# Performance work log

Measured on AMD Instinct MI355X. Metric: run time of the kernel, lower is better.

## Reference

```python
import jax, jax.numpy as jnp
from jax import lax
import numpy as np

T, B, I, H, OUT = 1024, 32, 128, 512, 10


def _lstm_layer(x, W_ih, W_hh, b):
    """PyTorch-convention LSTM layer. x: [T,B,in], W_ih: [4H,in], W_hh: [4H,H], b: [4H].
    Gate order: i, f, g, o. Returns all hidden states [T,B,H]."""
    hdim = W_hh.shape[1]
    # Precompute input projections for all timesteps (big GEMM, compute-bound).
    x_proj = jnp.einsum('tbi,gi->tbg', x, W_ih) + b  # [T,B,4H]

    def step(carry, xp_t):
        h, c = carry
        gates = xp_t + h @ W_hh.T  # [B,4H]
        i_g, f_g, g_g, o_g = jnp.split(gates, 4, axis=-1)
        i_g = jax.nn.sigmoid(i_g)
        f_g = jax.nn.sigmoid(f_g)
        g_g = jnp.tanh(g_g)
        o_g = jax.nn.sigmoid(o_g)
        c = f_g * c + i_g * g_g
        h = o_g * jnp.tanh(c)
        return (h, c), h

    h0 = jnp.zeros((x.shape[1], hdim), x.dtype)
    c0 = jnp.zeros((x.shape[1], hdim), x.dtype)
    _, hs = lax.scan(step, (h0, c0), x_proj)
    return hs  # [T,B,H]


def setup_inputs() -> dict:
    key = jax.random.key(0)
    ks = jax.random.split(key, 9)
    s1 = 1.0 / np.sqrt(H)  # PyTorch LSTM init scale U(-1/sqrt(H), 1/sqrt(H)); use scaled normal
    return {
        'data': jax.random.normal(ks[0], (T, B, I), jnp.float32),
        'W_ih1': jax.random.normal(ks[1], (4 * H, I), jnp.float32) * s1,
        'W_hh1': jax.random.normal(ks[2], (4 * H, H), jnp.float32) * s1,
        'b1': jax.random.normal(ks[3], (4 * H,), jnp.float32) * s1,
        'W_ih2': jax.random.normal(ks[4], (4 * H, H), jnp.float32) * s1,
        'W_hh2': jax.random.normal(ks[5], (4 * H, H), jnp.float32) * s1,
        'b2': jax.random.normal(ks[6], (4 * H,), jnp.float32) * s1,
        'W3': jax.random.normal(ks[7], (OUT, H), jnp.float32) * s1,
        'b3': jax.random.normal(ks[8], (OUT,), jnp.float32) * s1,
    }


def reference(data, W_ih1, W_hh1, b1, W_ih2, W_hh2, b2, W3, b3):
    h = _lstm_layer(data, W_ih1, W_hh1, b1)   # [T,B,H]
    h = _lstm_layer(h, W_ih2, W_hh2, b2)      # [T,B,H]
    logits = jnp.einsum('tbh,oh->tbo', h, W3) + b3  # [T,B,OUT]
    return jax.nn.softmax(logits, axis=2)
```

## Files before the change

kernel.cpp:

```cpp
#include <hip/hip_runtime.h>
#include <cstdint>
#include <cstddef>

#define TCHUNK 128
#define NCHUNK 8
#define BATCH 32
#define IDIM 128
#define HDIM 512
#define GDIM 2048
#define ODIM 10
#define NBLK 256
#define XPSTEP (GDIM * BATCH)
#define SLAB_F 16384
#define SLAB_B (SLAB_F * 4)

typedef float f4 __attribute__((ext_vector_type(4)));
typedef float f2 __attribute__((ext_vector_type(2)));

__device__ __forceinline__ void llc_store(float* p, float v) {
  asm volatile("global_store_dword %0, %1, off sc0 sc1" :: "v"(p), "v"(v) : "memory");
}
__device__ __forceinline__ float quad_sum(float x) {
  int t = __builtin_amdgcn_update_dpp(0, __float_as_int(x), 0xB1, 0xF, 0xF, true);
  x += __int_as_float(t);
  t = __builtin_amdgcn_update_dpp(0, __float_as_int(x), 0x4E, 0xF, 0xF, true);
  x += __int_as_float(t);
  return x;
}

#define BARRIER() do {                                                      \
    asm volatile("s_waitcnt lgkmcnt(0)" ::: "memory");                      \
    __builtin_amdgcn_sched_barrier(0);                                      \
    __builtin_amdgcn_s_barrier();                                           \
    __builtin_amdgcn_sched_barrier(0);                                      \
  } while (0)

template<int K>
__launch_bounds__(256, 2)
__global__ void proj_kernel(const float* __restrict__ X,
                            const float* __restrict__ W,
                            const float* __restrict__ bias,
                            float* __restrict__ P) {
  __shared__ float Xs[8][132];
  __shared__ float Ws[8][132];
  const int tid = threadIdx.x;
  const int n0 = blockIdx.x * 128;
  const int m0 = blockIdx.y * 128;
  const int tx = tid & 15, ty = tid >> 4;
  const int lm = tid >> 1;
  const int kq = (tid & 1) * 4;
  f2 acc2[8][4];
#pragma unroll
  for (int i = 0; i < 8; ++i)
#pragma unroll
    for (int j = 0; j < 4; ++j) acc2[i][j] = (f2){0.f, 0.f};

  for (int k0 = 0; k0 < K; k0 += 8) {
    const float4 xv = *(const float4*)&X[(size_t)(m0 + lm) * K + k0 + kq];
    const float4 wv = *(const float4*)&W[(size_t)(n0 + lm) * K + k0 + kq];
    __syncthreads();
    Xs[kq + 0][lm] = xv.x; Xs[kq + 1][lm] = xv.y; Xs[kq + 2][lm] = xv.z; Xs[kq + 3][lm] = xv.w;
    Ws[kq + 0][lm] = wv.x; Ws[kq + 1][lm] = wv.y; Ws[kq + 2][lm] = wv.z; Ws[kq + 3][lm] = wv.w;
    __syncthreads();
#pragma unroll
    for (int kk = 0; kk < 8; ++kk) {
      float a[8];
      *(float4*)&a[0] = *(const float4*)&Xs[kk][ty * 8];
      *(float4*)&a[4] = *(const float4*)&Xs[kk][ty * 8 + 4];
      f2 b2[4];
#pragma unroll
      for (int jp = 0; jp < 4; ++jp) b2[jp] = *(const f2*)&Ws[kk][tx * 8 + 2 * jp];
#pragma unroll
      for (int i = 0; i < 8; ++i)
#pragma unroll
        for (int jp = 0; jp < 4; ++jp) acc2[i][jp] += b2[jp] * a[i];
    }
  }
  const int mb = m0 + ty * 8;
  const int t  = mb >> 5;
  const int b0 = mb & 31;
#pragma unroll
  for (int j = 0; j < 8; ++j) {
    const int n = n0 + tx * 8 + j;
    const float bj = bias[n];
    float* dst = &P[((size_t)t * GDIM + n) * BATCH + b0];
#pragma unroll
    for (int i = 0; i < 8; ++i)
      dst[i] = ((j & 1) ? acc2[i][j >> 1].y : acc2[i][j >> 1].x) + bj;
  }
}

__launch_bounds__(256, 1)
__global__ void scan_kernel(const float* __restrict__ xp,
                            const float* __restrict__ Whh,
                            float* __restrict__ hout,
                            float* __restrict__ hb,
                            float* __restrict__ ccur,
                            int first) {
  __shared__ float h_s[2112];
  __shared__ float red[1024];
  __shared__ float gate_s[256];
  __shared__ float pad[17408];

  const int tid = threadIdx.x, bid = blockIdx.x;
  const int g = bid & 7, rank = bid >> 3, slot16 = rank * 16;
  const int w = tid >> 6, l = tid & 63;
  const int s4 = l & 3, rq = l >> 2;
  const int sg = 4 * w + s4;
  const int cx = sg & 7;
  const int kb = 32 * sg;

  float wreg[4][32];
#pragma unroll
  for (int r = 0; r < 4; ++r) {
    const int rl = 4 * rq + r;
    const float* wp = Whh + (size_t)((rl >> 4) * HDIM + slot16 + (rl & 15)) * HDIM + kb;
#pragma unroll
    for (int e = 0; e < 32; ++e) wreg[r][e] = wp[e ^ cx];
  }

  const int cl = l >> 4, m = l & 15;
  const int sgS = 4 * w + (m >> 2);
  const int sig = sgS & 7;
  int dsaddr[8];
#pragma unroll
  for (int i = 0; i < 8; ++i)
    dsaddr[i] = 132 * sgS + 4 * (8 * (m & 3) + (i ^ sig)) + cl;
  const int srcoff = cl * 512 + 128 * w + 8 * m;

  const int qg = tid >> 6, jg = (tid >> 2) & 15, bg = tid & 3;
  const float* xq = xp + (size_t)(qg * HDIM + slot16 + jg) * BATCH + g * 4 + bg;

  const int jj = l >> 2, bb = l & 3;

  float c_st = 0.f;
  if (!first && w == 0) c_st = ccur[(size_t)(g * 4 + bb) * HDIM + slot16 + jj];

  const float* hptr = &h_s[132 * sg];

#pragma unroll 1
  for (int tt = 0; tt < TCHUNK; ++tt) {
    const float* src = hb + (size_t)tt * SLAB_F + g * 2048 + srcoff;
    f4 va, vb;
    int guard = 0;
    while (true) {
      asm volatile("global_load_dwordx4 %0, %2, off sc0 sc1\n\t"
                   "global_load_dwordx4 %1, %3, off sc0 sc1\n\t"
                   "s_waitcnt vmcnt(0)"
                   : "=&v"(va), "=&v"(vb) : "v"(src), "v"(src + 4) : "memory");
      const bool ok =
          __float_as_uint(va.x) != 0xFFFFFFFFu && __float_as_uint(va.y) != 0xFFFFFFFFu &&
          __float_as_uint(va.z) != 0xFFFFFFFFu && __float_as_uint(va.w) != 0xFFFFFFFFu &&
          __float_as_uint(vb.x) != 0xFFFFFFFFu && __float_as_uint(vb.y) != 0xFFFFFFFFu &&
          __float_as_uint(vb.z) != 0xFFFFFFFFu && __float_as_uint(vb.w) != 0xFFFFFFFFu;
      if (__all(ok) || ++guard > 100000) break;
      __builtin_amdgcn_s_sleep(1);
    }
    h_s[dsaddr[0]] = va.x; h_s[dsaddr[1]] = va.y;
    h_s[dsaddr[2]] = va.z; h_s[dsaddr[3]] = va.w;
    h_s[dsaddr[4]] = vb.x; h_s[dsaddr[5]] = vb.y;
    h_s[dsaddr[6]] = vb.z; h_s[dsaddr[7]] = vb.w;
    const float xpv = xq[(size_t)tt * XPSTEP];
    BARRIER();

    f2 a01[4], a23[4];
#pragma unroll
    for (int r = 0; r < 4; ++r) { a01[r] = (f2){0.f, 0.f}; a23[r] = (f2){0.f, 0.f}; }
#pragma unroll
    for (int kk = 0; kk < 32; ++kk) {
      const f4 hv = *(const f4*)&hptr[4 * kk];
      const f2 h01 = {hv.x, hv.y}, h23 = {hv.z, hv.w};
#pragma unroll
      for (int r = 0; r < 4; ++r) {
        a01[r] += h01 * wreg[r][kk];
        a23[r] += h23 * wreg[r][kk];
      }
    }
#pragma unroll
    for (int r = 0; r < 4; ++r) {
      a01[r].x = quad_sum(a01[r].x); a01[r].y = quad_sum(a01[r].y);
      a23[r].x = quad_sum(a23[r].x); a23[r].y = quad_sum(a23[r].y);
    }
    f2 r01, r23;
    { const f2 v0 = (s4 & 1) ? a01[1] : a01[0];
      const f2 v1 = (s4 & 1) ? a01[3] : a01[2];
      r01 = (s4 & 2) ? v1 : v0;
      const f2 u0 = (s4 & 1) ? a23[1] : a23[0];
      const f2 u1 = (s4 & 1) ? a23[3] : a23[2];
      r23 = (s4 & 2) ? u1 : u0; }
    *(f4*)&red[(w << 8) + 4 * l] = (f4){r01.x, r01.y, r23.x, r23.y};
    BARRIER();

    const float pre = red[tid] + red[256 + tid] + red[512 + tid] + red[768 + tid] + xpv;
    gate_s[tid] = (qg == 2) ? tanhf(pre) : 1.f / (1.f + __expf(-pre));
    BARRIER();

    if (w == 0) {
      const float ig = gate_s[jj * 4 + bb];
      const float fg = gate_s[64 + jj * 4 + bb];
      const float gg = gate_s[128 + jj * 4 + bb];
      const float og = gate_s[192 + jj * 4 + bb];
      c_st = fg * c_st + ig * gg;
      const float hval = og * tanhf(c_st);
      llc_store(hb + (size_t)(tt + 1) * SLAB_F + g * 2048 + bb * 512 + slot16 + jj, hval);
      hout[(size_t)tt * (BATCH * HDIM) + (size_t)(g * 4 + bb) * HDIM + slot16 + jj] = hval;
    }
  }
  if (w == 0) ccur[(size_t)(g * 4 + bb) * HDIM + slot16 + jj] = c_st;
  ((volatile float*)pad)[tid] = c_st;
}

__launch_bounds__(256, 2)
__global__ void head_kernel(const float* __restrict__ h2,
                            const float* __restrict__ W3,
                            const float* __restrict__ b3,
                            float* __restrict__ outp) {
  const int tid = threadIdx.x;
  const int lane = tid & 63;
  const int wv = tid >> 6;
  const int row = blockIdx.x * 4 + wv;
  const float* hrow = &h2[(size_t)row * HDIM];
  float hreg[8];
  *(float4*)&hreg[0] = *(const float4*)&hrow[lane * 8];
  *(float4*)&hreg[4] = *(const float4*)&hrow[lane * 8 + 4];
  float logit[ODIM];
#pragma unroll
  for (int o = 0; o < ODIM; ++o) {
    const float* wrow = &W3[o * HDIM + lane * 8];
    float w[8];
    *(float4*)&w[0] = *(const float4*)&wrow[0];
    *(float4*)&w[4] = *(const float4*)&wrow[4];
    float pp = 0.f;
#pragma unroll
    for (int j = 0; j < 8; ++j) pp += hreg[j] * w[j];
#pragma unroll
    for (int off = 32; off > 0; off >>= 1) pp += __shfl_xor(pp, off);
    logit[o] = pp + b3[o];
  }
  float mx = logit[0];
#pragma unroll
  for (int o = 1; o < ODIM; ++o) mx = fmaxf(mx, logit[o]);
  float ssum = 0.f;
#pragma unroll
  for (int o = 0; o < ODIM; ++o) { logit[o] = __expf(logit[o] - mx); ssum += logit[o]; }
  const float inv = 1.f / ssum;
  if (lane == 0) {
    float* dst = &outp[(size_t)row * ODIM];
#pragma unroll
    for (int o = 0; o < ODIM; ++o) dst[o] = logit[o] * inv;
  }
}

extern "C" void kernel_launch(void* const* d_in, const int* in_sizes, int n_in,
                              void* d_out, int out_size, void* d_ws, size_t ws_size,
                              hipStream_t stream) {
  const float* data  = (const float*)d_in[0];
  const float* W_ih1 = (const float*)d_in[1];
  const float* W_hh1 = (const float*)d_in[2];
  const float* b1    = (const float*)d_in[3];
  const float* W_ih2 = (const float*)d_in[4];
  const float* W_hh2 = (const float*)d_in[5];
  const float* b2    = (const float*)d_in[6];
  const float* W3    = (const float*)d_in[7];
  const float* b3    = (const float*)d_in[8];
  float* outp = (float*)d_out;

  char* ws = (char*)d_ws;
  size_t off = 0;
  float* xp    = (float*)(ws + off); off += (size_t)TCHUNK * GDIM * BATCH * 4;
  float* h1c   = (float*)(ws + off); off += (size_t)TCHUNK * BATCH * HDIM * 4;
  float* h2c   = (float*)(ws + off); off += (size_t)TCHUNK * BATCH * HDIM * 4;
  float* hb1   = (float*)(ws + off); off += (size_t)(TCHUNK + 1) * SLAB_B;
  float* hb2   = (float*)(ws + off); off += (size_t)(TCHUNK + 1) * SLAB_B;
  float* ccur1 = (float*)(ws + off); off += BATCH * HDIM * 4;
  float* ccur2 = (float*)(ws + off); off += BATCH * HDIM * 4;
  if (off > ws_size) return;

  hipMemsetAsync(hb1, 0x00, SLAB_B, stream);
  hipMemsetAsync((char*)hb1 + SLAB_B, 0xFF, (size_t)TCHUNK * SLAB_B, stream);
  hipMemsetAsync(hb2, 0x00, SLAB_B, stream);
  hipMemsetAsync((char*)hb2 + SLAB_B, 0xFF, (size_t)TCHUNK * SLAB_B, stream);

  const dim3 pgrid(GDIM / 128, (TCHUNK * BATCH) / 128);
  for (int c = 0; c < NCHUNK; ++c) {
    const float* xin = data + (size_t)c * TCHUNK * BATCH * IDIM;
    proj_kernel<IDIM><<<pgrid, 256, 0, stream>>>(xin, W_ih1, b1, xp);
    scan_kernel<<<NBLK, 256, 0, stream>>>(xp, W_hh1, h1c, hb1, ccur1, c == 0);
    if (c < NCHUNK - 1) {
      hipMemcpyAsync(hb1, (char*)hb1 + (size_t)TCHUNK * SLAB_B, SLAB_B,
                     hipMemcpyDeviceToDevice, stream);
      hipMemsetAsync((char*)hb1 + SLAB_B, 0xFF, (size_t)TCHUNK * SLAB_B, stream);
    }
    proj_kernel<HDIM><<<pgrid, 256, 0, stream>>>(h1c, W_ih2, b2, xp);
    scan_kernel<<<NBLK, 256, 0, stream>>>(xp, W_hh2, h2c, hb2, ccur2, c == 0);
    if (c < NCHUNK - 1) {
      hipMemcpyAsync(hb2, (char*)hb2 + (size_t)TCHUNK * SLAB_B, SLAB_B,
                     hipMemcpyDeviceToDevice, stream);
      hipMemsetAsync((char*)hb2 + SLAB_B, 0xFF, (size_t)TCHUNK * SLAB_B, stream);
    }
    head_kernel<<<(TCHUNK * BATCH) / 4, 256, 0, stream>>>(
        h2c, W3, b3, outp + (size_t)c * TCHUNK * BATCH * ODIM);
  }
}
```

Before: 8.744 ms.

## Wavefront-pipeline both LSTM layers in one fused persistent scan kernel

Merges the two layer scans into one templated kernel that runs layer 1 on chunk c+1 and layer 2 on chunk c in the same timestep loop. Both layers share the barriers and the polling latency of each serial step. The chunk length is halved so the pipeline fill and drain are shorter, and a second xp buffer lets both projections stay live at once. In exchange each CU holds twice the recurrent weights in registers and does two dot phases per step, and there are more kernel launches and recycle memsets.

```diff
diff --git a/kernel.cpp b/kernel.cpp
--- a/kernel.cpp
+++ b/kernel.cpp
@@ -2,8 +2,8 @@
 #include <cstdint>
 #include <cstddef>
 
-#define TCHUNK 128
-#define NCHUNK 8
+#define TCHUNK 64
+#define NCHUNK 16
 #define BATCH 32
 #define IDIM 128
 #define HDIM 512
@@ -34,6 +34,11 @@
     __builtin_amdgcn_s_barrier();                                           \
     __builtin_amdgcn_sched_barrier(0);                                      \
   } while (0)
+
+#define SENT_OK(v) (__float_as_uint(v.x) != 0xFFFFFFFFu && \
+                    __float_as_uint(v.y) != 0xFFFFFFFFu && \
+                    __float_as_uint(v.z) != 0xFFFFFFFFu && \
+                    __float_as_uint(v.w) != 0xFFFFFFFFu)
 
 template<int K>
 __launch_bounds__(256, 2)
@@ -90,17 +95,21 @@
   }
 }
 
+template<bool L1, bool L2>
 __launch_bounds__(256, 1)
-__global__ void scan_kernel(const float* __restrict__ xp,
-                            const float* __restrict__ Whh,
-                            float* __restrict__ hout,
-                            float* __restrict__ hb,
-                            float* __restrict__ ccur,
-                            int first) {
-  __shared__ float h_s[2112];
-  __shared__ float red[1024];
-  __shared__ float gate_s[256];
-  __shared__ float pad[17408];
+__global__ void scan_pair(const float* __restrict__ xpA, const float* __restrict__ WhhA,
+                          float* __restrict__ houtA, float* __restrict__ hbA,
+                          float* __restrict__ ccurA, int firstA,
+                          const float* __restrict__ xpB, const float* __restrict__ WhhB,
+                          float* __restrict__ houtB, float* __restrict__ hbB,
+                          float* __restrict__ ccurB, int firstB) {
+  __shared__ float h_s1[2112];
+  __shared__ float h_s2[2112];
+  __shared__ float red1[1024];
+  __shared__ float red2[1024];
+  __shared__ float gate1[256];
+  __shared__ float gate2[256];
+  __shared__ float pad[13952];
 
   const int tid = threadIdx.x, bid = blockIdx.x;
   const int g = bid & 7, rank = bid >> 3, slot16 = rank * 16;
@@ -110,13 +119,24 @@
   const int cx = sg & 7;
   const int kb = 32 * sg;
 
-  float wreg[4][32];
-#pragma unroll
-  for (int r = 0; r < 4; ++r) {
-    const int rl = 4 * rq + r;
-    const float* wp = Whh + (size_t)((rl >> 4) * HDIM + slot16 + (rl & 15)) * HDIM + kb;
-#pragma unroll
-    for (int e = 0; e < 32; ++e) wreg[r][e] = wp[e ^ cx];
+  float wregA[4][32], wregB[4][32];
+  if constexpr (L1) {
+#pragma unroll
+    for (int r = 0; r < 4; ++r) {
+      const int rl = 4 * rq + r;
+      const float* wp = WhhA + (size_t)((rl >> 4) * HDIM + slot16 + (rl & 15)) * HDIM + kb;
+#pragma unroll
+      for (int e = 0; e < 32; ++e) wregA[r][e] = wp[e ^ cx];
+    }
+  }
+  if constexpr (L2) {
+#pragma unroll
+    for (int r = 0; r < 4; ++r) {
+      const int rl = 4 * rq + r;
+      const float* wp = WhhB + (size_t)((rl >> 4) * HDIM + slot16 + (rl & 15)) * HDIM + kb;
+#pragma unroll
+      for (int e = 0; e < 32; ++e) wregB[r][e] = wp[e ^ cx];
+    }
   }
 
   const int cl = l >> 4, m = l & 15;
@@ -129,85 +149,143 @@
   const int srcoff = cl * 512 + 128 * w + 8 * m;
 
   const int qg = tid >> 6, jg = (tid >> 2) & 15, bg = tid & 3;
-  const float* xq = xp + (size_t)(qg * HDIM + slot16 + jg) * BATCH + g * 4 + bg;
+  const size_t xqo = (size_t)(qg * HDIM + slot16 + jg) * BATCH + g * 4 + bg;
 
   const int jj = l >> 2, bb = l & 3;
-
-  float c_st = 0.f;
-  if (!first && w == 0) c_st = ccur[(size_t)(g * 4 + bb) * HDIM + slot16 + jj];
-
-  const float* hptr = &h_s[132 * sg];
+  const size_t cco = (size_t)(g * 4 + bb) * HDIM + slot16 + jj;
+
+  float cA = 0.f, cB = 0.f;
+  if (w == 0) {
+    if (L1 && !firstA) cA = ccurA[cco];
+    if (L2 && !firstB) cB = ccurB[cco];
+  }
+
+  const float* hp1 = &h_s1[132 * sg];
+  const float* hp2 = &h_s2[132 * sg];
 
 #pragma unroll 1
   for (int tt = 0; tt < TCHUNK; ++tt) {
-    const float* src = hb + (size_t)tt * SLAB_F + g * 2048 + srcoff;
-    f4 va, vb;
+    const float* s1 = hbA + (size_t)tt * SLAB_F + g * 2048 + srcoff;
+    const float* s2 = hbB + (size_t)tt * SLAB_F + g * 2048 + srcoff;
+    f4 va1, vb1, va2, vb2;
     int guard = 0;
     while (true) {
-      asm volatile("global_load_dwordx4 %0, %2, off sc0 sc1\n\t"
-                   "global_load_dwordx4 %1, %3, off sc0 sc1\n\t"
-                   "s_waitcnt vmcnt(0)"
-                   : "=&v"(va), "=&v"(vb) : "v"(src), "v"(src + 4) : "memory");
-      const bool ok =
-          __float_as_uint(va.x) != 0xFFFFFFFFu && __float_as_uint(va.y) != 0xFFFFFFFFu &&
-          __float_as_uint(va.z) != 0xFFFFFFFFu && __float_as_uint(va.w) != 0xFFFFFFFFu &&
-          __float_as_uint(vb.x) != 0xFFFFFFFFu && __float_as_uint(vb.y) != 0xFFFFFFFFu &&
-          __float_as_uint(vb.z) != 0xFFFFFFFFu && __float_as_uint(vb.w) != 0xFFFFFFFFu;
-      if (__all(ok) || ++guard > 100000) break;
+      bool ok;
+      if constexpr (L1 && L2) {
+        asm volatile("global_load_dwordx4 %0, %4, off sc0 sc1\n\t"
+                     "global_load_dwordx4 %1, %5, off sc0 sc1\n\t"
+                     "global_load_dwordx4 %2, %6, off sc0 sc1\n\t"
+                     "global_load_dwordx4 %3, %7, off sc0 sc1\n\t"
+                     "s_waitcnt vmcnt(0)"
+                     : "=&v"(va1), "=&v"(vb1), "=&v"(va2), "=&v"(vb2)
+                     : "v"(s1), "v"(s1 + 4), "v"(s2), "v"(s2 + 4) : "memory");
+        ok = SENT_OK(va1) && SENT_OK(vb1) && SENT_OK(va2) && SENT_OK(vb2);
+      } else if constexpr (L1) {
+        asm volatile("global_load_dwordx4 %0, %2, off sc0 sc1\n\t"
+                     "global_load_dwordx4 %1, %3, off sc0 sc1\n\t"
+                     "s_waitcnt vmcnt(0)"
+                     : "=&v"(va1), "=&v"(vb1) : "v"(s1), "v"(s1 + 4) : "memory");
+        ok = SENT_OK(va1) && SENT_OK(vb1);
+      } else {
+        asm volatile("global_load_dwordx4 %0, %2, off sc0 sc1\n\t"
+                     "global_load_dwordx4 %1, %3, off sc0 sc1\n\t"
+                     "s_waitcnt vmcnt(0)"
+                     : "=&v"(va2), "=&v"(vb2) : "v"(s2), "v"(s2 + 4) : "memory");
+        ok = SENT_OK(va2) && SENT_OK(vb2);
+      }
+      if (__all(ok) || ++guard > 200000) break;
       __builtin_amdgcn_s_sleep(1);
     }
-    h_s[dsaddr[0]] = va.x; h_s[dsaddr[1]] = va.y;
-    h_s[dsaddr[2]] = va.z; h_s[dsaddr[3]] = va.w;
-    h_s[dsaddr[4]] = vb.x; h_s[dsaddr[5]] = vb.y;
-    h_s[dsaddr[6]] = vb.z; h_s[dsaddr[7]] = vb.w;
-    const float xpv = xq[(size_t)tt * XPSTEP];
+    if constexpr (L1) {
+      h_s1[dsaddr[0]] = va1.x; h_s1[dsaddr[1]] = va1.y;
+      h_s1[dsaddr[2]] = va1.z; h_s1[dsaddr[3]] = va1.w;
+      h_s1[dsaddr[4]] = vb1.x; h_s1[dsaddr[5]] = vb1.y;
+      h_s1[dsaddr[6]] = vb1.z; h_s1[dsaddr[7]] = vb1.w;
+    }
+    if constexpr (L2) {
+      h_s2[dsaddr[0]] = va2.x; h_s2[dsaddr[1]] = va2.y;
+      h_s2[dsaddr[2]] = va2.z; h_s2[dsaddr[3]] = va2.w;
+      h_s2[dsaddr[4]] = vb2.x; h_s2[dsaddr[5]] = vb2.y;
+      h_s2[dsaddr[6]] = vb2.z; h_s2[dsaddr[7]] = vb2.w;
+    }
+    float xpv1 = 0.f, xpv2 = 0.f;
+    if constexpr (L1) xpv1 = xpA[(size_t)tt * XPSTEP + xqo];
+    if constexpr (L2) xpv2 = xpB[(size_t)tt * XPSTEP + xqo];
     BARRIER();
 
-    f2 a01[4], a23[4];
-#pragma unroll
-    for (int r = 0; r < 4; ++r) { a01[r] = (f2){0.f, 0.f}; a23[r] = (f2){0.f, 0.f}; }
-#pragma unroll
-    for (int kk = 0; kk < 32; ++kk) {
-      const f4 hv = *(const f4*)&hptr[4 * kk];
-      const f2 h01 = {hv.x, hv.y}, h23 = {hv.z, hv.w};
-#pragma unroll
-      for (int r = 0; r < 4; ++r) {
-        a01[r] += h01 * wreg[r][kk];
-        a23[r] += h23 * wreg[r][kk];
+#define DOT_PHASE(HPTR, WREG, RED)                                          \
+    {                                                                       \
+      f2 a01[4], a23[4];                                                    \
+      _Pragma("unroll")                                                     \
+      for (int r = 0; r < 4; ++r) { a01[r] = (f2){0.f,0.f}; a23[r] = (f2){0.f,0.f}; } \
+      _Pragma("unroll")                                                     \
+      for (int kk = 0; kk < 32; ++kk) {                                     \
+        const f4 hv = *(const f4*)&HPTR[4 * kk];                            \
+        const f2 h01 = {hv.x, hv.y}, h23 = {hv.z, hv.w};                    \
+        _Pragma("unroll")                                                   \
+        for (int r = 0; r < 4; ++r) {                                       \
+          a01[r] += h01 * WREG[r][kk];                                      \
+          a23[r] += h23 * WREG[r][kk];                                      \
+        }                                                                   \
+      }                                                                     \
+      _Pragma("unroll")                                                     \
+      for (int r = 0; r < 4; ++r) {                                         \
+        a01[r].x = quad_sum(a01[r].x); a01[r].y = quad_sum(a01[r].y);       \
+        a23[r].x = quad_sum(a23[r].x); a23[r].y = quad_sum(a23[r].y);       \
+      }                                                                     \
+      f2 r01, r23;                                                          \
+      { const f2 v0 = (s4 & 1) ? a01[1] : a01[0];                           \
+        const f2 v1 = (s4 & 1) ? a01[3] : a01[2];                           \
+        r01 = (s4 & 2) ? v1 : v0;                                           \
+        const f2 u0 = (s4 & 1) ? a23[1] : a23[0];                           \
+        const f2 u1 = (s4 & 1) ? a23[3] : a23[2];                           \
+        r23 = (s4 & 2) ? u1 : u0; }                                         \
+      *(f4*)&RED[(w << 8) + 4 * l] = (f4){r01.x, r01.y, r23.x, r23.y};      \
+    }
+
+    if constexpr (L1) DOT_PHASE(hp1, wregA, red1)
+    if constexpr (L2) DOT_PHASE(hp2, wregB, red2)
+    BARRIER();
+
+    if constexpr (L1) {
+      const float pre = red1[tid] + red1[256 + tid] + red1[512 + tid] + red1[768 + tid] + xpv1;
+      gate1[tid] = (qg == 2) ? tanhf(pre) : 1.f / (1.f + __expf(-pre));
+    }
+    if constexpr (L2) {
+      const float pre = red2[tid] + red2[256 + tid] + red2[512 + tid] + red2[768 + tid] + xpv2;
+      gate2[tid] = (qg == 2) ? tanhf(pre) : 1.f / (1.f + __expf(-pre));
+    }
+    BARRIER();
+
+    if (w == 0) {
+      if constexpr (L1) {
+        const float ig = gate1[jj * 4 + bb];
+        const float fg = gate1[64 + jj * 4 + bb];
+        const float gg = gate1[128 + jj * 4 + bb];
+        const float og = gate1[192 + jj * 4 + bb];
+        cA = fg * cA + ig * gg;
+        const float hval = og * tanhf(cA);
+        llc_store(hbA + (size_t)(tt + 1) * SLAB_F + g * 2048 + bb * 512 + slot16 + jj, hval);
+        houtA[(size_t)tt * (BATCH * HDIM) + cco] = hval;
       }
-    }
-#pragma unroll
-    for (int r = 0; r < 4; ++r) {
-      a01[r].x = quad_sum(a01[r].x); a01[r].y = quad_sum(a01[r].y);
-      a23[r].x = quad_sum(a23[r].x); a23[r].y = quad_sum(a23[r].y);
-    }
-    f2 r01, r23;
-    { const f2 v0 = (s4 & 1) ? a01[1] : a01[0];
-      const f2 v1 = (s4 & 1) ? a01[3] : a01[2];
-      r01 = (s4 & 2) ? v1 : v0;
-      const f2 u0 = (s4 & 1) ? a23[1] : a23[0];
-      const f2 u1 = (s4 & 1) ? a23[3] : a23[2];
-      r23 = (s4 & 2) ? u1 : u0; }
-    *(f4*)&red[(w << 8) + 4 * l] = (f4){r01.x, r01.y, r23.x, r23.y};
-    BARRIER();
-
-    const float pre = red[tid] + red[256 + tid] + red[512 + tid] + red[768 + tid] + xpv;
-    gate_s[tid] = (qg == 2) ? tanhf(pre) : 1.f / (1.f + __expf(-pre));
-    BARRIER();
-
-    if (w == 0) {
-      const float ig = gate_s[jj * 4 + bb];
-      const float fg = gate_s[64 + jj * 4 + bb];
-      const float gg = gate_s[128 + jj * 4 + bb];
-      const float og = gate_s[192 + jj * 4 + bb];
-      c_st = fg * c_st + ig * gg;
-      const float hval = og * tanhf(c_st);
-      llc_store(hb + (size_t)(tt + 1) * SLAB_F + g * 2048 + bb * 512 + slot16 + jj, hval);
-      hout[(size_t)tt * (BATCH * HDIM) + (size_t)(g * 4 + bb) * HDIM + slot16 + jj] = hval;
-    }
-  }
-  if (w == 0) ccur[(size_t)(g * 4 + bb) * HDIM + slot16 + jj] = c_st;
-  ((volatile float*)pad)[tid] = c_st;
+      if constexpr (L2) {
+        const float ig = gate2[jj * 4 + bb];
+        const float fg = gate2[64 + jj * 4 + bb];
+        const float gg = gate2[128 + jj * 4 + bb];
+        const float og = gate2[192 + jj * 4 + bb];
+        cB = fg * cB + ig * gg;
+        const float hval = og * tanhf(cB);
+        llc_store(hbB + (size_t)(tt + 1) * SLAB_F + g * 2048 + bb * 512 + slot16 + jj, hval);
+        houtB[(size_t)tt * (BATCH * HDIM) + cco] = hval;
+      }
+    }
+#undef DOT_PHASE
+  }
+  if (w == 0) {
+    if constexpr (L1) ccurA[cco] = cA;
+    if constexpr (L2) ccurB[cco] = cB;
+  }
+  ((volatile float*)pad)[tid] = cA + cB;
 }
 
 __launch_bounds__(256, 2)
@@ -267,7 +345,8 @@
 
   char* ws = (char*)d_ws;
   size_t off = 0;
-  float* xp    = (float*)(ws + off); off += (size_t)TCHUNK * GDIM * BATCH * 4;
+  float* xp1   = (float*)(ws + off); off += (size_t)TCHUNK * GDIM * BATCH * 4;
+  float* xp2   = (float*)(ws + off); off += (size_t)TCHUNK * GDIM * BATCH * 4;
   float* h1c   = (float*)(ws + off); off += (size_t)TCHUNK * BATCH * HDIM * 4;
   float* h2c   = (float*)(ws + off); off += (size_t)TCHUNK * BATCH * HDIM * 4;
   float* hb1   = (float*)(ws + off); off += (size_t)(TCHUNK + 1) * SLAB_B;
@@ -282,23 +361,38 @@
   hipMemsetAsync((char*)hb2 + SLAB_B, 0xFF, (size_t)TCHUNK * SLAB_B, stream);
 
   const dim3 pgrid(GDIM / 128, (TCHUNK * BATCH) / 128);
-  for (int c = 0; c < NCHUNK; ++c) {
-    const float* xin = data + (size_t)c * TCHUNK * BATCH * IDIM;
-    proj_kernel<IDIM><<<pgrid, 256, 0, stream>>>(xin, W_ih1, b1, xp);
-    scan_kernel<<<NBLK, 256, 0, stream>>>(xp, W_hh1, h1c, hb1, ccur1, c == 0);
-    if (c < NCHUNK - 1) {
-      hipMemcpyAsync(hb1, (char*)hb1 + (size_t)TCHUNK * SLAB_B, SLAB_B,
-                     hipMemcpyDeviceToDevice, stream);
-      hipMemsetAsync((char*)hb1 + SLAB_B, 0xFF, (size_t)TCHUNK * SLAB_B, stream);
-    }
-    proj_kernel<HDIM><<<pgrid, 256, 0, stream>>>(h1c, W_ih2, b2, xp);
-    scan_kernel<<<NBLK, 256, 0, stream>>>(xp, W_hh2, h2c, hb2, ccur2, c == 0);
-    if (c < NCHUNK - 1) {
-      hipMemcpyAsync(hb2, (char*)hb2 + (size_t)TCHUNK * SLAB_B, SLAB_B,
-                     hipMemcpyDeviceToDevice, stream);
-      hipMemsetAsync((char*)hb2 + SLAB_B, 0xFF, (size_t)TCHUNK * SLAB_B, stream);
-    }
+
+#define RECYCLE(HB) do {                                                    \
+    hipMemcpyAsync(HB, (char*)HB + (size_t)TCHUNK * SLAB_B, SLAB_B,         \
+                   hipMemcpyDeviceToDevice, stream);                        \
+    hipMemsetAsync((char*)HB + SLAB_B, 0xFF, (size_t)TCHUNK * SLAB_B, stream); \
+  } while (0)
+
+  proj_kernel<IDIM><<<pgrid, 256, 0, stream>>>(data, W_ih1, b1, xp1);
+  scan_pair<true, false><<<NBLK, 256, 0, stream>>>(
+      xp1, W_hh1, h1c, hb1, ccur1, 1, xp2, W_hh2, h2c, hb2, ccur2, 1);
+  RECYCLE(hb1);
+  proj_kernel<HDIM><<<pgrid, 256, 0, stream>>>(h1c, W_ih2, b2, xp2);
+  proj_kernel<IDIM><<<pgrid, 256, 0, stream>>>(
+      data + (size_t)TCHUNK * BATCH * IDIM, W_ih1, b1, xp1);
+
+  for (int c = 0; c < NCHUNK - 1; ++c) {
+    scan_pair<true, true><<<NBLK, 256, 0, stream>>>(
+        xp1, W_hh1, h1c, hb1, ccur1, 0,
+        xp2, W_hh2, h2c, hb2, ccur2, c == 0);
     head_kernel<<<(TCHUNK * BATCH) / 4, 256, 0, stream>>>(
         h2c, W3, b3, outp + (size_t)c * TCHUNK * BATCH * ODIM);
-  }
-}
+    RECYCLE(hb1);
+    RECYCLE(hb2);
+    proj_kernel<HDIM><<<pgrid, 256, 0, stream>>>(h1c, W_ih2, b2, xp2);
+    if (c + 2 < NCHUNK)
+      proj_kernel<IDIM><<<pgrid, 256, 0, stream>>>(
+          data + (size_t)(c + 2) * TCHUNK * BATCH * IDIM, W_ih1, b1, xp1);
+  }
+
+  scan_pair<false, true><<<NBLK, 256, 0, stream>>>(
+      xp1, W_hh1, h1c, hb1, ccur1, 0, xp2, W_hh2, h2c, hb2, ccur2, 0);
+  head_kernel<<<(TCHUNK * BATCH) / 4, 256, 0, stream>>>(
+      h2c, W3, b3, outp + (size_t)(NCHUNK - 1) * TCHUNK * BATCH * ODIM);
+#undef RECYCLE
+}
```

New measurement: 13.75 ms. 1.57x slower.

## Wavefront-pipeline both LSTM layers in one split scan kernel

Applied to the files above, without the earlier changes.

Merges the two layer scans into one launch. Layer 2 processes chunk s-1 while layer 1 processes chunk s, each on half the blocks (128 per layer). Each block now owns 32 hidden units and holds twice as many recurrent weights in registers. The chunk size is halved to shorten the pipeline fill. The aim is to overlap the two serial recurrences and roughly halve the total serial step count. The cost is twice the per-block dot-product work per step, much higher register pressure, and more launches and memset/copy traffic per chunk.

```diff
diff --git a/kernel.cpp b/kernel.cpp
--- a/kernel.cpp
+++ b/kernel.cpp
@@ -2,8 +2,8 @@
 #include <cstdint>
 #include <cstddef>
 
-#define TCHUNK 128
-#define NCHUNK 8
+#define TCHUNK 64
+#define NCHUNK 16
 #define BATCH 32
 #define IDIM 128
 #define HDIM 512
@@ -91,32 +91,45 @@
 }
 
 __launch_bounds__(256, 1)
-__global__ void scan_kernel(const float* __restrict__ xp,
-                            const float* __restrict__ Whh,
-                            float* __restrict__ hout,
-                            float* __restrict__ hb,
-                            float* __restrict__ ccur,
-                            int first) {
+__global__ void scan_split(const float* __restrict__ xp1, const float* __restrict__ Whh1,
+                           float* __restrict__ hout1, float* __restrict__ hb1,
+                           float* __restrict__ ccur1, int first1, int act1,
+                           const float* __restrict__ xp2, const float* __restrict__ Whh2,
+                           float* __restrict__ hout2, float* __restrict__ hb2,
+                           float* __restrict__ ccur2, int first2, int act2) {
   __shared__ float h_s[2112];
-  __shared__ float red[1024];
-  __shared__ float gate_s[256];
-  __shared__ float pad[17408];
-
-  const int tid = threadIdx.x, bid = blockIdx.x;
-  const int g = bid & 7, rank = bid >> 3, slot16 = rank * 16;
+  __shared__ float red[2048];
+  __shared__ float gate_s[512];
+  __shared__ float pad[15872];
+
+  const int bid = blockIdx.x;
+  const int lay = bid >> 7;
+  if (!(lay ? act2 : act1)) return;
+  const float* xp  = lay ? xp2  : xp1;
+  const float* Whh = lay ? Whh2 : Whh1;
+  float* hout = lay ? hout2 : hout1;
+  float* hb   = lay ? hb2   : hb1;
+  float* ccur = lay ? ccur2 : ccur1;
+  const int first = lay ? first2 : first1;
+
+  const int tid = threadIdx.x;
+  const int bidl = bid & 127;
+  const int g = bidl & 7, rank = bidl >> 3, slot32 = rank * 32;
   const int w = tid >> 6, l = tid & 63;
   const int s4 = l & 3, rq = l >> 2;
   const int sg = 4 * w + s4;
   const int cx = sg & 7;
   const int kb = 32 * sg;
 
-  float wreg[4][32];
+  float wA[4][32], wB[4][32];
 #pragma unroll
   for (int r = 0; r < 4; ++r) {
     const int rl = 4 * rq + r;
-    const float* wp = Whh + (size_t)((rl >> 4) * HDIM + slot16 + (rl & 15)) * HDIM + kb;
-#pragma unroll
-    for (int e = 0; e < 32; ++e) wreg[r][e] = wp[e ^ cx];
+    const int s = rl & 31;
+    const float* wpA = Whh + (size_t)((rl >> 5) * HDIM + slot32 + s) * HDIM + kb;
+    const float* wpB = Whh + (size_t)((2 + (rl >> 5)) * HDIM + slot32 + s) * HDIM + kb;
+#pragma unroll
+    for (int e = 0; e < 32; ++e) { wA[r][e] = wpA[e ^ cx]; wB[r][e] = wpB[e ^ cx]; }
   }
 
   const int cl = l >> 4, m = l & 15;
@@ -128,13 +141,17 @@
     dsaddr[i] = 132 * sgS + 4 * (8 * (m & 3) + (i ^ sig)) + cl;
   const int srcoff = cl * 512 + 128 * w + 8 * m;
 
-  const int qg = tid >> 6, jg = (tid >> 2) & 15, bg = tid & 3;
-  const float* xq = xp + (size_t)(qg * HDIM + slot16 + jg) * BATCH + g * 4 + bg;
-
-  const int jj = l >> 2, bb = l & 3;
+  const int rowA = tid >> 2, chn = tid & 3;
+  const size_t xqoA = (size_t)((rowA >> 5) * HDIM + slot32 + (rowA & 31)) * BATCH
+                      + g * 4 + chn;
+  const size_t xqoB = xqoA + (size_t)2 * HDIM * BATCH;
+
+  const int uj = ((w << 6) + l) >> 2;
+  const int ub = l & 3;
+  const size_t cco = (size_t)(g * 4 + ub) * HDIM + slot32 + uj;
 
   float c_st = 0.f;
-  if (!first && w == 0) c_st = ccur[(size_t)(g * 4 + bb) * HDIM + slot16 + jj];
+  if (!first && w < 2) c_st = ccur[cco];
 
   const float* hptr = &h_s[132 * sg];
 
@@ -153,60 +170,73 @@
           __float_as_uint(va.z) != 0xFFFFFFFFu && __float_as_uint(va.w) != 0xFFFFFFFFu &&
           __float_as_uint(vb.x) != 0xFFFFFFFFu && __float_as_uint(vb.y) != 0xFFFFFFFFu &&
           __float_as_uint(vb.z) != 0xFFFFFFFFu && __float_as_uint(vb.w) != 0xFFFFFFFFu;
-      if (__all(ok) || ++guard > 100000) break;
+      if (__all(ok) || ++guard > 200000) break;
       __builtin_amdgcn_s_sleep(1);
     }
     h_s[dsaddr[0]] = va.x; h_s[dsaddr[1]] = va.y;
     h_s[dsaddr[2]] = va.z; h_s[dsaddr[3]] = va.w;
     h_s[dsaddr[4]] = vb.x; h_s[dsaddr[5]] = vb.y;
     h_s[dsaddr[6]] = vb.z; h_s[dsaddr[7]] = vb.w;
-    const float xpv = xq[(size_t)tt * XPSTEP];
+    const float xpvA = xp[(size_t)tt * XPSTEP + xqoA];
+    const float xpvB = xp[(size_t)tt * XPSTEP + xqoB];
     BARRIER();
 
-    f2 a01[4], a23[4];
-#pragma unroll
-    for (int r = 0; r < 4; ++r) { a01[r] = (f2){0.f, 0.f}; a23[r] = (f2){0.f, 0.f}; }
-#pragma unroll
-    for (int kk = 0; kk < 32; ++kk) {
-      const f4 hv = *(const f4*)&hptr[4 * kk];
-      const f2 h01 = {hv.x, hv.y}, h23 = {hv.z, hv.w};
-#pragma unroll
-      for (int r = 0; r < 4; ++r) {
-        a01[r] += h01 * wreg[r][kk];
-        a23[r] += h23 * wreg[r][kk];
-      }
-    }
-#pragma unroll
-    for (int r = 0; r < 4; ++r) {
-      a01[r].x = quad_sum(a01[r].x); a01[r].y = quad_sum(a01[r].y);
-      a23[r].x = quad_sum(a23[r].x); a23[r].y = quad_sum(a23[r].y);
-    }
-    f2 r01, r23;
-    { const f2 v0 = (s4 & 1) ? a01[1] : a01[0];
-      const f2 v1 = (s4 & 1) ? a01[3] : a01[2];
-      r01 = (s4 & 2) ? v1 : v0;
-      const f2 u0 = (s4 & 1) ? a23[1] : a23[0];
-      const f2 u1 = (s4 & 1) ? a23[3] : a23[2];
-      r23 = (s4 & 2) ? u1 : u0; }
-    *(f4*)&red[(w << 8) + 4 * l] = (f4){r01.x, r01.y, r23.x, r23.y};
+#define DOT_BANK(WREG, ROFF)                                                \
+    {                                                                       \
+      f2 a01[4], a23[4];                                                    \
+      _Pragma("unroll")                                                     \
+      for (int r = 0; r < 4; ++r) { a01[r] = (f2){0.f,0.f}; a23[r] = (f2){0.f,0.f}; } \
+      _Pragma("unroll")                                                     \
+      for (int kk = 0; kk < 32; ++kk) {                                     \
+        const f4 hv = *(const f4*)&hptr[4 * kk];                            \
+        const f2 h01 = {hv.x, hv.y}, h23 = {hv.z, hv.w};                    \
+        _Pragma("unroll")                                                   \
+        for (int r = 0; r < 4; ++r) {                                       \
+          a01[r] += h01 * WREG[r][kk];                                      \
+          a23[r] += h23 * WREG[r][kk];                                      \
+        }                                                                   \
+      }                                                                     \
+      _Pragma("unroll")                                                     \
+      for (int r = 0; r < 4; ++r) {                                         \
+        a01[r].x = quad_sum(a01[r].x); a01[r].y = quad_sum(a01[r].y);       \
+        a23[r].x = quad_sum(a23[r].x); a23[r].y = quad_sum(a23[r].y);       \
+      }                                                                     \
+      f2 r01, r23;                                                          \
+      { const f2 v0 = (s4 & 1) ? a01[1] : a01[0];                           \
+        const f2 v1 = (s4 & 1) ? a01[3] : a01[2];                           \
+        r01 = (s4 & 2) ? v1 : v0;                                           \
+        const f2 u0 = (s4 & 1) ? a23[1] : a23[0];                           \
+        const f2 u1 = (s4 & 1) ? a23[3] : a23[2];                           \
+        r23 = (s4 & 2) ? u1 : u0; }                                         \
+      *(f4*)&red[(ROFF) + (w << 8) + 4 * l] = (f4){r01.x, r01.y, r23.x, r23.y}; \
+    }
+    DOT_BANK(wA, 0)
+    DOT_BANK(wB, 1024)
+#undef DOT_BANK
     BARRIER();
 
-    const float pre = red[tid] + red[256 + tid] + red[512 + tid] + red[768 + tid] + xpv;
-    gate_s[tid] = (qg == 2) ? tanhf(pre) : 1.f / (1.f + __expf(-pre));
+    {
+      const float preA = red[tid] + red[256 + tid] + red[512 + tid] + red[768 + tid] + xpvA;
+      gate_s[tid] = 1.f / (1.f + __expf(-preA));
+      const float preB = red[1024 + tid] + red[1280 + tid] + red[1536 + tid]
+                       + red[1792 + tid] + xpvB;
+      gate_s[256 + tid] = (tid < 128) ? tanhf(preB)
+                                      : 1.f / (1.f + __expf(-preB));
+    }
     BARRIER();
 
-    if (w == 0) {
-      const float ig = gate_s[jj * 4 + bb];
-      const float fg = gate_s[64 + jj * 4 + bb];
-      const float gg = gate_s[128 + jj * 4 + bb];
-      const float og = gate_s[192 + jj * 4 + bb];
+    if (w < 2) {
+      const float ig = gate_s[uj * 4 + ub];
+      const float fg = gate_s[128 + uj * 4 + ub];
+      const float gg = gate_s[256 + uj * 4 + ub];
+      const float og = gate_s[384 + uj * 4 + ub];
       c_st = fg * c_st + ig * gg;
       const float hval = og * tanhf(c_st);
-      llc_store(hb + (size_t)(tt + 1) * SLAB_F + g * 2048 + bb * 512 + slot16 + jj, hval);
-      hout[(size_t)tt * (BATCH * HDIM) + (size_t)(g * 4 + bb) * HDIM + slot16 + jj] = hval;
-    }
-  }
-  if (w == 0) ccur[(size_t)(g * 4 + bb) * HDIM + slot16 + jj] = c_st;
+      llc_store(hb + (size_t)(tt + 1) * SLAB_F + g * 2048 + ub * 512 + slot32 + uj, hval);
+      hout[(size_t)tt * (BATCH * HDIM) + cco] = hval;
+    }
+  }
+  if (w < 2) ccur[cco] = c_st;
   ((volatile float*)pad)[tid] = c_st;
 }
 
@@ -267,7 +297,8 @@
 
   char* ws = (char*)d_ws;
   size_t off = 0;
-  float* xp    = (float*)(ws + off); off += (size_t)TCHUNK * GDIM * BATCH * 4;
+  float* xp1   = (float*)(ws + off); off += (size_t)TCHUNK * GDIM * BATCH * 4;
+  float* xp2   = (float*)(ws + off); off += (size_t)TCHUNK * GDIM * BATCH * 4;
   float* h1c   = (float*)(ws + off); off += (size_t)TCHUNK * BATCH * HDIM * 4;
   float* h2c   = (float*)(ws + off); off += (size_t)TCHUNK * BATCH * HDIM * 4;
   float* hb1   = (float*)(ws + off); off += (size_t)(TCHUNK + 1) * SLAB_B;
@@ -282,23 +313,33 @@
   hipMemsetAsync((char*)hb2 + SLAB_B, 0xFF, (size_t)TCHUNK * SLAB_B, stream);
 
   const dim3 pgrid(GDIM / 128, (TCHUNK * BATCH) / 128);
-  for (int c = 0; c < NCHUNK; ++c) {
-    const float* xin = data + (size_t)c * TCHUNK * BATCH * IDIM;
-    proj_kernel<IDIM><<<pgrid, 256, 0, stream>>>(xin, W_ih1, b1, xp);
-    scan_kernel<<<NBLK, 256, 0, stream>>>(xp, W_hh1, h1c, hb1, ccur1, c == 0);
-    if (c < NCHUNK - 1) {
-      hipMemcpyAsync(hb1, (char*)hb1 + (size_t)TCHUNK * SLAB_B, SLAB_B,
-                     hipMemcpyDeviceToDevice, stream);
-      hipMemsetAsync((char*)hb1 + SLAB_B, 0xFF, (size_t)TCHUNK * SLAB_B, stream);
-    }
-    proj_kernel<HDIM><<<pgrid, 256, 0, stream>>>(h1c, W_ih2, b2, xp);
-    scan_kernel<<<NBLK, 256, 0, stream>>>(xp, W_hh2, h2c, hb2, ccur2, c == 0);
-    if (c < NCHUNK - 1) {
-      hipMemcpyAsync(hb2, (char*)hb2 + (size_t)TCHUNK * SLAB_B, SLAB_B,
-                     hipMemcpyDeviceToDevice, stream);
-      hipMemsetAsync((char*)hb2 + SLAB_B, 0xFF, (size_t)TCHUNK * SLAB_B, stream);
-    }
-    head_kernel<<<(TCHUNK * BATCH) / 4, 256, 0, stream>>>(
-        h2c, W3, b3, outp + (size_t)c * TCHUNK * BATCH * ODIM);
-  }
-}
+
+#define RECYCLE(HB) do {                                                    \
+    hipMemcpyAsync(HB, (char*)HB + (size_t)TCHUNK * SLAB_B, SLAB_B,         \
+                   hipMemcpyDeviceToDevice, stream);                        \
+    hipMemsetAsync((char*)HB + SLAB_B, 0xFF, (size_t)TCHUNK * SLAB_B, stream); \
+  } while (0)
+
+  proj_kernel<IDIM><<<pgrid, 256, 0, stream>>>(data, W_ih1, b1, xp1);
+
+  for (int s = 0; s <= NCHUNK; ++s) {
+    const int act1 = (s < NCHUNK);
+    const int act2 = (s >= 1);
+    scan_split<<<NBLK, 256, 0, stream>>>(
+        xp1, W_hh1, h1c, hb1, ccur1, s == 0, act1,
+        xp2, W_hh2, h2c, hb2, ccur2, s == 1, act2);
+    if (act1) {
+      RECYCLE(hb1);
+      proj_kernel<HDIM><<<pgrid, 256, 0, stream>>>(h1c, W_ih2, b2, xp2);
+      if (s + 1 < NCHUNK)
+        proj_kernel<IDIM><<<pgrid, 256, 0, stream>>>(
+            data + (size_t)(s + 1) * TCHUNK * BATCH * IDIM, W_ih1, b1, xp1);
+    }
+    if (act2) {
+      if (s < NCHUNK) RECYCLE(hb2);
+      head_kernel<<<(TCHUNK * BATCH) / 4, 256, 0, stream>>>(
+          h2c, W3, b3, outp + (size_t)(s - 1) * TCHUNK * BATCH * ODIM);
+    }
+  }
+#undef RECYCLE
+}
```

Measured after the change: 11.38 ms. 1.3x slower.

## Pipeline both LSTM layers' scans concurrently in one dual-layer kernel launch

Applied to the files above, without the earlier changes.

The two separate layer scans are merged into one kernel of 512 blocks. The first 256 blocks run layer 1 on chunk s while the other 256 run layer 2 on chunk s-1, so the two recurrences overlap instead of running back to back. Chunk size is halved to shorten pipeline fill, and the padding shared buffer that forced one block per CU is removed so two blocks can share a CU. Separate xp buffers let the projections for the next step be computed between launches. The trade-off is co-resident blocks competing for CU resources and spin-wait correctness depending on all 512 blocks being resident at once.

```diff
diff --git a/kernel.cpp b/kernel.cpp
--- a/kernel.cpp
+++ b/kernel.cpp
@@ -2,14 +2,13 @@
 #include <cstdint>
 #include <cstddef>
 
-#define TCHUNK 128
-#define NCHUNK 8
+#define TCHUNK 64
+#define NCHUNK 16
 #define BATCH 32
 #define IDIM 128
 #define HDIM 512
 #define GDIM 2048
 #define ODIM 10
-#define NBLK 256
 #define XPSTEP (GDIM * BATCH)
 #define SLAB_F 16384
 #define SLAB_B (SLAB_F * 4)
@@ -90,20 +89,30 @@
   }
 }
 
-__launch_bounds__(256, 1)
-__global__ void scan_kernel(const float* __restrict__ xp,
-                            const float* __restrict__ Whh,
-                            float* __restrict__ hout,
-                            float* __restrict__ hb,
-                            float* __restrict__ ccur,
-                            int first) {
+__launch_bounds__(256, 2)
+__global__ void scan_dual(const float* __restrict__ xp1, const float* __restrict__ Whh1,
+                          float* __restrict__ hout1, float* __restrict__ hb1,
+                          float* __restrict__ ccur1, int first1, int act1,
+                          const float* __restrict__ xp2, const float* __restrict__ Whh2,
+                          float* __restrict__ hout2, float* __restrict__ hb2,
+                          float* __restrict__ ccur2, int first2, int act2) {
   __shared__ float h_s[2112];
   __shared__ float red[1024];
   __shared__ float gate_s[256];
-  __shared__ float pad[17408];
-
-  const int tid = threadIdx.x, bid = blockIdx.x;
-  const int g = bid & 7, rank = bid >> 3, slot16 = rank * 16;
+
+  const int bid = blockIdx.x;
+  const int lay = bid >> 8;
+  if (!(lay ? act2 : act1)) return;
+  const float* xp  = lay ? xp2  : xp1;
+  const float* Whh = lay ? Whh2 : Whh1;
+  float* hout = lay ? hout2 : hout1;
+  float* hb   = lay ? hb2   : hb1;
+  float* ccur = lay ? ccur2 : ccur1;
+  const int first = lay ? first2 : first1;
+
+  const int tid = threadIdx.x;
+  const int bidl = bid & 255;
+  const int g = bidl & 7, rank = bidl >> 3, slot16 = rank * 16;
   const int w = tid >> 6, l = tid & 63;
   const int s4 = l & 3, rq = l >> 2;
   const int sg = 4 * w + s4;
@@ -153,7 +162,7 @@
           __float_as_uint(va.z) != 0xFFFFFFFFu && __float_as_uint(va.w) != 0xFFFFFFFFu &&
           __float_as_uint(vb.x) != 0xFFFFFFFFu && __float_as_uint(vb.y) != 0xFFFFFFFFu &&
           __float_as_uint(vb.z) != 0xFFFFFFFFu && __float_as_uint(vb.w) != 0xFFFFFFFFu;
-      if (__all(ok) || ++guard > 100000) break;
+      if (__all(ok) || ++guard > 200000) break;
       __builtin_amdgcn_s_sleep(1);
     }
     h_s[dsaddr[0]] = va.x; h_s[dsaddr[1]] = va.y;
@@ -207,7 +216,6 @@
     }
   }
   if (w == 0) ccur[(size_t)(g * 4 + bb) * HDIM + slot16 + jj] = c_st;
-  ((volatile float*)pad)[tid] = c_st;
 }
 
 __launch_bounds__(256, 2)
@@ -267,7 +275,8 @@
 
   char* ws = (char*)d_ws;
   size_t off = 0;
-  float* xp    = (float*)(ws + off); off += (size_t)TCHUNK * GDIM * BATCH * 4;
+  float* xp1   = (float*)(ws + off); off += (size_t)TCHUNK * GDIM * BATCH * 4;
+  float* xp2   = (float*)(ws + off); off += (size_t)TCHUNK * GDIM * BATCH * 4;
   float* h1c   = (float*)(ws + off); off += (size_t)TCHUNK * BATCH * HDIM * 4;
   float* h2c   = (float*)(ws + off); off += (size_t)TCHUNK * BATCH * HDIM * 4;
   float* hb1   = (float*)(ws + off); off += (size_t)(TCHUNK + 1) * SLAB_B;
@@ -282,23 +291,33 @@
   hipMemsetAsync((char*)hb2 + SLAB_B, 0xFF, (size_t)TCHUNK * SLAB_B, stream);
 
   const dim3 pgrid(GDIM / 128, (TCHUNK * BATCH) / 128);
-  for (int c = 0; c < NCHUNK; ++c) {
-    const float* xin = data + (size_t)c * TCHUNK * BATCH * IDIM;
-    proj_kernel<IDIM><<<pgrid, 256, 0, stream>>>(xin, W_ih1, b1, xp);
-    scan_kernel<<<NBLK, 256, 0, stream>>>(xp, W_hh1, h1c, hb1, ccur1, c == 0);
-    if (c < NCHUNK - 1) {
-      hipMemcpyAsync(hb1, (char*)hb1 + (size_t)TCHUNK * SLAB_B, SLAB_B,
-                     hipMemcpyDeviceToDevice, stream);
-      hipMemsetAsync((char*)hb1 + SLAB_B, 0xFF, (size_t)TCHUNK * SLAB_B, stream);
-    }
-    proj_kernel<HDIM><<<pgrid, 256, 0, stream>>>(h1c, W_ih2, b2, xp);
-    scan_kernel<<<NBLK, 256, 0, stream>>>(xp, W_hh2, h2c, hb2, ccur2, c == 0);
-    if (c < NCHUNK - 1) {
-      hipMemcpyAsync(hb2, (char*)hb2 + (size_t)TCHUNK * SLAB_B, SLAB_B,
-                     hipMemcpyDeviceToDevice, stream);
-      hipMemsetAsync((char*)hb2 + SLAB_B, 0xFF, (size_t)TCHUNK * SLAB_B, stream);
-    }
-    head_kernel<<<(TCHUNK * BATCH) / 4, 256, 0, stream>>>(
-        h2c, W3, b3, outp + (size_t)c * TCHUNK * BATCH * ODIM);
-  }
-}
+
+#define RECYCLE(HB) do {                                                    \
+    hipMemcpyAsync(HB, (char*)HB + (size_t)TCHUNK * SLAB_B, SLAB_B,         \
+                   hipMemcpyDeviceToDevice, stream);                        \
+    hipMemsetAsync((char*)HB + SLAB_B, 0xFF, (size_t)TCHUNK * SLAB_B, stream); \
+  } while (0)
+
+  proj_kernel<IDIM><<<pgrid, 256, 0, stream>>>(data, W_ih1, b1, xp1);
+
+  for (int s = 0; s <= NCHUNK; ++s) {
+    const int act1 = (s < NCHUNK);
+    const int act2 = (s >= 1);
+    scan_dual<<<512, 256, 0, stream>>>(
+        xp1, W_hh1, h1c, hb1, ccur1, s == 0, act1,
+        xp2, W_hh2, h2c, hb2, ccur2, s == 1, act2);
+    if (act1) {
+      RECYCLE(hb1);
+      proj_kernel<HDIM><<<pgrid, 256, 0, stream>>>(h1c, W_ih2, b2, xp2);
+      if (s + 1 < NCHUNK)
+        proj_kernel<IDIM><<<pgrid, 256, 0, stream>>>(
+            data + (size_t)(s + 1) * TCHUNK * BATCH * IDIM, W_ih1, b1, xp1);
+    }
+    if (act2) {
+      if (s < NCHUNK) RECYCLE(hb2);
+      head_kernel<<<(TCHUNK * BATCH) / 4, 256, 0, stream>>>(
+          h2c, W3, b3, outp + (size_t)(s - 1) * TCHUNK * BATCH * ODIM);
+    }
+  }
+#undef RECYCLE
+}
```

Result: slower. 12.03 ms (+37.6%).
